# Performance work log

Hardware: AMD Instinct MI355X
Metric: run time of the kernel (lower is better)

## Reference

```python
import jax, jax.numpy as jnp
import numpy as np

HEAD_DIM = 128
MAX_TIMESCALE = 10000.0
MIN_TIMESCALE = 1.0


def _rope(x, pos):
    # x: [B, S, H, D], pos: [B, S]
    d = x.shape[-1]
    fraction = 2.0 * jnp.arange(0, d // 2, dtype=jnp.float32) / d
    timescale = MIN_TIMESCALE * (MAX_TIMESCALE / MIN_TIMESCALE) ** fraction  # [D/2]
    sinusoid = pos.astype(jnp.float32)[..., None, None] / timescale  # [B,S,1,D/2]
    sin, cos = jnp.sin(sinusoid), jnp.cos(sinusoid)
    xf = x.astype(jnp.float32)
    x1, x2 = jnp.split(xf, 2, axis=-1)
    return jnp.concatenate((x1 * cos - x2 * sin, x2 * cos + x1 * sin), axis=-1).astype(x.dtype)


def setup_inputs() -> dict:
    key = jax.random.key(0)
    ks = jax.random.split(key, 5)
    B, T, D, N, K, H = 2, 2048, 2048, 16, 4, HEAD_DIM
    s = 0.02
    X = jax.random.normal(ks[0], (B, T, D), dtype=jnp.float32)
    q_positions = jnp.broadcast_to(jnp.arange(T, dtype=jnp.int32), (B, T))
    Wq = jax.random.normal(ks[1], (D, N, H), dtype=jnp.float32) * s
    Wk = jax.random.normal(ks[2], (D, K, H), dtype=jnp.float32) * s
    Wv = jax.random.normal(ks[3], (D, K, H), dtype=jnp.float32) * s
    Wo = jax.random.normal(ks[4], (N, H, D), dtype=jnp.float32) * s
    return {"X": X, "q_positions": q_positions, "Wq": Wq, "Wk": Wk, "Wv": Wv, "Wo": Wo}


def reference(X, q_positions, Wq, Wk, Wv, Wo):
    B, T, D = X.shape
    N, K = Wq.shape[1], Wk.shape[1]
    groups = N // K
    # fused QKV projections (DenseGeneral, no bias)
    q = jnp.einsum('btd,dnh->btnh', X, Wq)  # [B,T,N,H]
    k = jnp.einsum('btd,dkh->btkh', X, Wk)  # [B,T,K,H]
    v = jnp.einsum('btd,dkh->btkh', X, Wv)  # [B,T,K,H]
    # RoPE (note: original uses q_positions sin/cos for both q and k in the no-cache path)
    q = _rope(q, q_positions)
    k = _rope(k, q_positions)
    # GQA: broadcast kv heads to query heads
    k = jnp.repeat(k, groups, axis=2)  # [B,T,N,H]
    v = jnp.repeat(v, groups, axis=2)
    # attention with scale=1.0 and causal masking
    scores = jnp.einsum('btnh,bsnh->bnts', q, k)  # [B,N,T,T]
    causal = jnp.tril(jnp.ones((T, T), dtype=bool))
    scores = jnp.where(causal, scores, jnp.finfo(scores.dtype).min)
    probs = jax.nn.softmax(scores, axis=-1)
    attn = jnp.einsum('bnts,bsnh->btnh', probs, v)  # [B,T,N,H]
    # output projection contracting (head, head_dim)
    out = jnp.einsum('btnh,nhd->btd', attn, Wo)
    return out.astype(X.dtype)
```

## Files before the change

kernel.cpp:

```cpp
#include <hip/hip_runtime.h>
#include <math.h>

#define DEVI static __device__ __forceinline__

using f16x8 = __attribute__((ext_vector_type(8))) _Float16;
using f32x4  = __attribute__((ext_vector_type(4))) float;

constexpr int Bb = 2, Tt = 2048, Dd = 2048, NQ = 16, NK = 4, HD = 128;
constexpr int Mrows = Bb * Tt;
constexpr int QKVC  = NQ*HD + 2*NK*HD;
constexpr int KOFF  = NQ*HD;
constexpr int VOFF  = NQ*HD + NK*HD;

DEVI ushort f2h(float f) {
  _Float16 h = (_Float16)f;
  union { _Float16 h; ushort u; } v; v.h = h;
  return v.u;
}
DEVI float h2f(ushort u) {
  union { ushort u; _Float16 h; } v; v.u = u;
  return (float)v.h;
}

typedef const __attribute__((address_space(1))) unsigned* gp1;
typedef __attribute__((address_space(3))) unsigned* lp3;
DEVI void gload16(void* lds, const void* g) {
  __builtin_amdgcn_global_load_lds((gp1)g, (lp3)lds, 16, 0, 0);
}

__global__ void k_cvt(const float* __restrict__ x, ushort* __restrict__ o, int n4) {
  int i = blockIdx.x * blockDim.x + threadIdx.x;
  if (i >= n4) return;
  float4 v = ((const float4*)x)[i];
  ushort4 u;
  u.x = f2h(v.x); u.y = f2h(v.y); u.z = f2h(v.z); u.w = f2h(v.w);
  ((ushort4*)o)[i] = u;
}

__global__ void k_tconv(const float* __restrict__ in, ushort* __restrict__ out, int R, int C) {
  __shared__ float t[32][33];
  const int c0 = blockIdx.x * 32, r0 = blockIdx.y * 32;
  const int tx = threadIdx.x, ty = threadIdx.y;
#pragma unroll
  for (int i = 0; i < 32; i += 8)
    t[ty + i][tx] = in[(size_t)(r0 + ty + i) * C + (c0 + tx)];
  __syncthreads();
#pragma unroll
  for (int i = 0; i < 32; i += 8)
    out[(size_t)(c0 + ty + i) * R + (r0 + tx)] = f2h(t[tx][ty + i]);
}

DEVI void stv(float* p, float v)  { *p = v; }
DEVI void stv(ushort* p, float v) { *p = f2h(v); }

template <typename OT>
__launch_bounds__(256)
__global__ void k_gemm_bt(const ushort* __restrict__ A, const ushort* __restrict__ Bt,
                          OT* __restrict__ C, int M, int N, int Kd) {
  __shared__ char As[8192];
  __shared__ char Bs[8192];
  const int tid = threadIdx.x;
  const int l = tid & 63, w = tid >> 6;
  const int wr = w >> 1, wc = w & 1;
  const int lr = l & 15, lk = l >> 4;
  const size_t row0 = (size_t)blockIdx.y * 128, col0 = (size_t)blockIdx.x * 128;

  f32x4 acc[4][4];
#pragma unroll
  for (int i = 0; i < 4; ++i)
#pragma unroll
    for (int j = 0; j < 4; ++j) acc[i][j] = (f32x4){0.f, 0.f, 0.f, 0.f};

  const int c0i = tid, c1i = tid + 256;
  const int ra0 = c0i >> 2, sa0 = (c0i & 3) ^ ((ra0 >> 1) & 3);
  const int ra1 = c1i >> 2, sa1 = (c1i & 3) ^ ((ra1 >> 1) & 3);

  for (int kt = 0; kt < Kd; kt += 32) {
    if (kt) __syncthreads();
    gload16(As + c0i * 16, A + (row0 + ra0) * Kd + kt + sa0 * 8);
    gload16(As + c1i * 16, A + (row0 + ra1) * Kd + kt + sa1 * 8);
    gload16(Bs + c0i * 16, Bt + (col0 + ra0) * Kd + kt + sa0 * 8);
    gload16(Bs + c1i * 16, Bt + (col0 + ra1) * Kd + kt + sa1 * 8);
    __syncthreads();
    f16x8 af[4], bfr[4];
#pragma unroll
    for (int i = 0; i < 4; ++i) {
      int ra = wr * 64 + i * 16 + lr;
      af[i] = *(const f16x8*)(As + ra * 64 + ((lk ^ ((ra >> 1) & 3)) << 4));
      int rb = wc * 64 + i * 16 + lr;
      bfr[i] = *(const f16x8*)(Bs + rb * 64 + ((lk ^ ((rb >> 1) & 3)) << 4));
    }
#pragma unroll
    for (int i = 0; i < 4; ++i)
#pragma unroll
      for (int j = 0; j < 4; ++j)
        acc[i][j] = __builtin_amdgcn_mfma_f32_16x16x32_f16(af[i], bfr[j], acc[i][j], 0, 0, 0);
  }
#pragma unroll
  for (int i = 0; i < 4; ++i) {
    size_t r = row0 + wr * 64 + i * 16 + lk * 4;
#pragma unroll
    for (int j = 0; j < 4; ++j) {
      size_t cc = col0 + wc * 64 + j * 16 + lr;
#pragma unroll
      for (int rg = 0; rg < 4; ++rg) stv(&C[(r + rg) * N + cc], acc[i][j][rg]);
    }
  }
}

__global__ void k_rope_tab(const int* __restrict__ pos, float* __restrict__ tab) {
  int idx = blockIdx.x * blockDim.x + threadIdx.x;
  if (idx >= Mrows * 64) return;
  int m = idx >> 6, i = idx & 63;
  double a = (double)pos[m] * exp2(-0.20762050593045952 * (double)i);
  tab[idx * 2]     = (float)cos(a);
  tab[idx * 2 + 1] = (float)sin(a);
}

__global__ void k_rope(ushort* __restrict__ qkv, const float* __restrict__ tab) {
  int idx = blockIdx.x * blockDim.x + threadIdx.x;
  if (idx >= Mrows * 20 * 8) return;
  int chunk = idx & 7;
  int h20 = (idx >> 3) % 20;
  int m = idx / 160;
  int colbase = (h20 < 16) ? h20 * 128 : (KOFF + (h20 - 16) * 128);
  size_t base = (size_t)m * QKVC + colbase + chunk * 8;
  union { uint4 v; ushort s[8]; } A1, A2, O1, O2;
  A1.v = *(const uint4*)(qkv + base);
  A2.v = *(const uint4*)(qkv + base + 64);
  const float* tp = tab + ((size_t)m * 64 + chunk * 8) * 2;
#pragma unroll
  for (int j = 0; j < 8; ++j) {
    float c = tp[2 * j], s = tp[2 * j + 1];
    float x1 = h2f(A1.s[j]), x2 = h2f(A2.s[j]);
    O1.s[j] = f2h(x1 * c - x2 * s);
    O2.s[j] = f2h(x2 * c + x1 * s);
  }
  *(uint4*)(qkv + base) = O1.v;
  *(uint4*)(qkv + base + 64) = O2.v;
}

__global__ void k_vt(const ushort* __restrict__ qkv, ushort* __restrict__ vt) {
  __shared__ ushort t[32][33];
  const int bg = blockIdx.z, bq = bg >> 2, g = bg & 3;
  const int s0 = blockIdx.x * 32, h0 = blockIdx.y * 32;
  const int tx = threadIdx.x, ty = threadIdx.y;
#pragma unroll
  for (int i = 0; i < 32; i += 8)
    t[ty + i][tx] = qkv[(size_t)(bq * Tt + s0 + ty + i) * QKVC + VOFF + g * HD + h0 + tx];
  __syncthreads();
#pragma unroll
  for (int i = 0; i < 32; i += 8)
    vt[((size_t)bg * HD + h0 + ty + i) * Tt + (s0 + tx)] = t[tx][ty + i];
}

__launch_bounds__(512, 4)
__global__ void k_flash(const ushort* __restrict__ qkv, const ushort* __restrict__ vt,
                        ushort* __restrict__ attn) {
  __shared__ char Ks[2][16384];
  __shared__ char Vs[2][16384];
  __shared__ char Pl[8][2048];
  const int b = blockIdx.x;
  const int vv = b >> 8, u = b & 255;
  const int hid = u >> 3, p = u & 7;
  const int qt = vv ? p : (15 - p);
  const int bq = hid >> 4, n = hid & 15, g = n >> 2;
  const int tid = threadIdx.x, w = tid >> 6, l = tid & 63;
  const int lr = l & 15, lk = l >> 4;
  const int t0 = qt * 128;
  const int qrow = t0 + w * 16;

  f16x8 qf[4];
  {
    const size_t qb = ((size_t)(bq * Tt + qrow + lr)) * QKVC + n * HD + lk * 8;
#pragma unroll
    for (int kt = 0; kt < 4; ++kt) qf[kt] = *(const f16x8*)(qkv + qb + kt * 32);
  }
  f32x4 O[8];
#pragma unroll
  for (int hb = 0; hb < 8; ++hb) O[hb] = (f32x4){0.f, 0.f, 0.f, 0.f};
  float mrow[4] = {-INFINITY, -INFINITY, -INFINITY, -INFINITY};
  float lrow[4] = {0.f, 0.f, 0.f, 0.f};

  const size_t kgbase = (size_t)(bq * Tt) * QKVC + KOFF + g * HD;
  const size_t vgbase = (size_t)(bq * 4 + g) * HD * Tt;
  const int ntiles = 2 * qt + 2;

  int srow[2], koin[2], hrow[2], voin[2];
#pragma unroll
  for (int cc = 0; cc < 2; ++cc) {
    int c = cc * 512 + tid;
    srow[cc] = c >> 4;
    koin[cc] = (((c & 15) << 4) ^ ((srow[cc] & 7) << 4)) >> 1;
    hrow[cc] = c >> 3;
    voin[cc] = (((c & 7) << 4) ^ ((hrow[cc] & 7) << 4)) >> 1;
  }

#define STAGE(buf, s0s)                                                              \
  {                                                                                  \
    _Pragma("unroll")                                                                \
    for (int cc = 0; cc < 2; ++cc) {                                                 \
      int c16 = (cc * 512 + tid) * 16;                                               \
      gload16(Ks[buf] + c16, qkv + kgbase + (size_t)((s0s) + srow[cc]) * QKVC + koin[cc]); \
      gload16(Vs[buf] + c16, vt + vgbase + (size_t)hrow[cc] * Tt + (s0s) + voin[cc]); \
    }                                                                                \
  }

  STAGE(0, 0);
  __syncthreads();

  for (int j = 0; j < ntiles; ++j) {
    const int cur = j & 1;
    if (j + 1 < ntiles) STAGE(cur ^ 1, (j + 1) * 64);
    const int s0 = j * 64;
    if (s0 <= qrow + 15) {
      f32x4 sc[4];
#pragma unroll
      for (int ns = 0; ns < 4; ++ns) {
        f32x4 a = (f32x4){0.f, 0.f, 0.f, 0.f};
        int sl = ns * 16 + lr;
#pragma unroll
        for (int kt = 0; kt < 4; ++kt) {
          int inner = (kt * 64 + lk * 16) ^ ((sl & 7) << 4);
          f16x8 kf = *(const f16x8*)(Ks[cur] + sl * 256 + inner);
          a = __builtin_amdgcn_mfma_f32_16x16x32_f16(qf[kt], kf, a, 0, 0, 0);
        }
        sc[ns] = a;
      }
      if (s0 + 63 > qrow) {
#pragma unroll
        for (int ns = 0; ns < 4; ++ns) {
          int scol = s0 + ns * 16 + lr;
#pragma unroll
          for (int r = 0; r < 4; ++r)
            if (scol > qrow + lk * 4 + r) sc[ns][r] = -INFINITY;
        }
      }
      float scl[4], rs[4];
#pragma unroll
      for (int r = 0; r < 4; ++r) {
        float v0 = fmaxf(fmaxf(sc[0][r], sc[1][r]), fmaxf(sc[2][r], sc[3][r]));
#pragma unroll
        for (int d = 1; d < 16; d <<= 1) v0 = fmaxf(v0, __shfl_xor(v0, d));
        float mn = fmaxf(mrow[r], v0);
        scl[r] = __expf(mrow[r] - mn);
        mrow[r] = mn;
        rs[r] = 0.f;
      }
#pragma unroll
      for (int ns = 0; ns < 4; ++ns)
#pragma unroll
        for (int r = 0; r < 4; ++r) {
          float pv = __expf(sc[ns][r] - mrow[r]);
          rs[r] += pv;
          int q = lk * 4 + r;
          *(ushort*)(Pl[w] + q * 128 + ((ns * 32 + lr * 2) ^ ((q & 7) << 4))) = f2h(pv);
        }
#pragma unroll
      for (int r = 0; r < 4; ++r) {
#pragma unroll
        for (int d = 1; d < 16; d <<= 1) rs[r] += __shfl_xor(rs[r], d);
        lrow[r] = lrow[r] * scl[r] + rs[r];
      }
#pragma unroll
      for (int hb = 0; hb < 8; ++hb)
#pragma unroll
        for (int r = 0; r < 4; ++r) O[hb][r] *= scl[r];
      const char* pb = Pl[w] + lr * 128;
      const int sw = (lr & 7) << 4;
      f16x8 pa0 = *(const f16x8*)(pb + ((lk * 16) ^ sw));
      f16x8 pa1 = *(const f16x8*)(pb + ((64 + lk * 16) ^ sw));
#pragma unroll
      for (int hb = 0; hb < 8; ++hb) {
        int h = hb * 16 + lr;
        int inner0 = (lk * 16) ^ ((h & 7) << 4);
        f16x8 vf0 = *(const f16x8*)(Vs[cur] + h * 128 + inner0);
        O[hb] = __builtin_amdgcn_mfma_f32_16x16x32_f16(pa0, vf0, O[hb], 0, 0, 0);
        int inner1 = (64 + lk * 16) ^ ((h & 7) << 4);
        f16x8 vf1 = *(const f16x8*)(Vs[cur] + h * 128 + inner1);
        O[hb] = __builtin_amdgcn_mfma_f32_16x16x32_f16(pa1, vf1, O[hb], 0, 0, 0);
      }
    }
    __syncthreads();
  }
#undef STAGE
  float inv[4];
#pragma unroll
  for (int r = 0; r < 4; ++r) inv[r] = 1.f / lrow[r];
#pragma unroll
  for (int hb = 0; hb < 8; ++hb)
#pragma unroll
    for (int r = 0; r < 4; ++r) {
      size_t orow = (size_t)(bq * Tt + qrow + lk * 4 + r);
      attn[orow * 2048 + n * HD + hb * 16 + lr] = f2h(O[hb][r] * inv[r]);
    }
}

extern "C" void kernel_launch(void* const* d_in, const int* in_sizes, int n_in,
                              void* d_out, int out_size, void* d_ws, size_t ws_size,
                              hipStream_t stream) {
  const float* X  = (const float*)d_in[0];
  const int*   qp = (const int*)d_in[1];
  const float* Wq = (const float*)d_in[2];
  const float* Wk = (const float*)d_in[3];
  const float* Wv = (const float*)d_in[4];
  const float* Wo = (const float*)d_in[5];
  float* out = (float*)d_out;
  char* ws = (char*)d_ws;

  ushort* Xf    = (ushort*)(ws + 0);
  ushort* WqkvT = (ushort*)(ws + 16777216);
  ushort* WoT   = (ushort*)(ws + 29360128);
  ushort* QKV   = (ushort*)(ws + 37748736);
  ushort* VT    = (ushort*)(ws + 62914560);
  ushort* attn  = (ushort*)(ws + 67108864);
  float*  tab   = (float*)(ws + 83886080);

  dim3 tb(32, 8);
  k_cvt<<<(Mrows * Dd / 4 + 255) / 256, 256, 0, stream>>>(X, Xf, Mrows * Dd / 4);
  k_tconv<<<dim3(64, 64), tb, 0, stream>>>(Wq, WqkvT, Dd, NQ * HD);
  k_tconv<<<dim3(16, 64), tb, 0, stream>>>(Wk, WqkvT + (size_t)KOFF * Dd, Dd, NK * HD);
  k_tconv<<<dim3(16, 64), tb, 0, stream>>>(Wv, WqkvT + (size_t)VOFF * Dd, Dd, NK * HD);
  k_tconv<<<dim3(64, 64), tb, 0, stream>>>(Wo, WoT, NQ * HD, Dd);
  k_gemm_bt<ushort><<<dim3(QKVC / 128, Mrows / 128), 256, 0, stream>>>(
      Xf, WqkvT, QKV, Mrows, QKVC, Dd);
  k_rope_tab<<<(Mrows * 64 + 255) / 256, 256, 0, stream>>>(qp, tab);
  k_rope<<<(Mrows * 160 + 255) / 256, 256, 0, stream>>>(QKV, tab);
  k_vt<<<dim3(Tt / 32, HD / 32, Bb * NK), tb, 0, stream>>>(QKV, VT);
  k_flash<<<dim3(512), 512, 0, stream>>>(QKV, VT, attn);
  k_gemm_bt<float><<<dim3(Dd / 128, Mrows / 128), 256, 0, stream>>>(
      attn, WoT, out, Mrows, Dd, Dd);
}
```

Baseline: 251.0 us.

## Transpose QK MFMA operands for lane-local softmax with lazy rescaling

Swaps the QK^T MFMA operands so each lane holds one query row's scores, which removes most of the cross-lane max and sum shuffles and allows packed fp16 stores of P into LDS. It adds a lazy online-softmax rescale that only updates the running max when a row's max grows by more than a threshold, so the O rescaling is usually skipped. It also adds s_setprio around the MFMA blocks and relaxes launch bounds from 4 to 2 waves per EU. The risks are lower occupancy and a round-toward-zero fp16 conversion of P with a stale max, where probabilities can reach up to e^8.

```diff
diff --git a/kernel.cpp b/kernel.cpp
--- a/kernel.cpp
+++ b/kernel.cpp
@@ -4,6 +4,7 @@
 #define DEVI static __device__ __forceinline__
 
 using f16x8 = __attribute__((ext_vector_type(8))) _Float16;
+using h16x2 = __attribute__((ext_vector_type(2))) __fp16;
 using f32x4  = __attribute__((ext_vector_type(4))) float;
 
 constexpr int Bb = 2, Tt = 2048, Dd = 2048, NQ = 16, NK = 4, HD = 128;
@@ -154,7 +155,7 @@
     vt[((size_t)bg * HD + h0 + ty + i) * Tt + (s0 + tx)] = t[tx][ty + i];
 }
 
-__launch_bounds__(512, 4)
+__launch_bounds__(512, 2)
 __global__ void k_flash(const ushort* __restrict__ qkv, const ushort* __restrict__ vt,
                         ushort* __restrict__ attn) {
   __shared__ char Ks[2][16384];
@@ -169,6 +170,7 @@
   const int lr = l & 15, lk = l >> 4;
   const int t0 = qt * 128;
   const int qrow = t0 + w * 16;
+  const int qglob = qrow + lr;
 
   f16x8 qf[4];
   {
@@ -179,8 +181,7 @@
   f32x4 O[8];
 #pragma unroll
   for (int hb = 0; hb < 8; ++hb) O[hb] = (f32x4){0.f, 0.f, 0.f, 0.f};
-  float mrow[4] = {-INFINITY, -INFINITY, -INFINITY, -INFINITY};
-  float lrow[4] = {0.f, 0.f, 0.f, 0.f};
+  float m = -INFINITY, lsum = 0.f;
 
   const size_t kgbase = (size_t)(bq * Tt) * QKVC + KOFF + g * HD;
   const size_t vgbase = (size_t)(bq * 4 + g) * HD * Tt;
@@ -215,6 +216,7 @@
     const int s0 = j * 64;
     if (s0 <= qrow + 15) {
       f32x4 sc[4];
+      __builtin_amdgcn_s_setprio(1);
 #pragma unroll
       for (int ns = 0; ns < 4; ++ns) {
         f32x4 a = (f32x4){0.f, 0.f, 0.f, 0.f};
@@ -223,53 +225,60 @@
         for (int kt = 0; kt < 4; ++kt) {
           int inner = (kt * 64 + lk * 16) ^ ((sl & 7) << 4);
           f16x8 kf = *(const f16x8*)(Ks[cur] + sl * 256 + inner);
-          a = __builtin_amdgcn_mfma_f32_16x16x32_f16(qf[kt], kf, a, 0, 0, 0);
+          a = __builtin_amdgcn_mfma_f32_16x16x32_f16(kf, qf[kt], a, 0, 0, 0);
         }
         sc[ns] = a;
       }
+      __builtin_amdgcn_s_setprio(0);
       if (s0 + 63 > qrow) {
 #pragma unroll
-        for (int ns = 0; ns < 4; ++ns) {
-          int scol = s0 + ns * 16 + lr;
+        for (int ns = 0; ns < 4; ++ns)
 #pragma unroll
           for (int r = 0; r < 4; ++r)
-            if (scol > qrow + lk * 4 + r) sc[ns][r] = -INFINITY;
-        }
-      }
-      float scl[4], rs[4];
-#pragma unroll
-      for (int r = 0; r < 4; ++r) {
-        float v0 = fmaxf(fmaxf(sc[0][r], sc[1][r]), fmaxf(sc[2][r], sc[3][r]));
-#pragma unroll
-        for (int d = 1; d < 16; d <<= 1) v0 = fmaxf(v0, __shfl_xor(v0, d));
-        float mn = fmaxf(mrow[r], v0);
-        scl[r] = __expf(mrow[r] - mn);
-        mrow[r] = mn;
-        rs[r] = 0.f;
-      }
+            if (s0 + ns * 16 + lk * 4 + r > qglob) sc[ns][r] = -INFINITY;
+      }
+      float pm = -INFINITY;
 #pragma unroll
       for (int ns = 0; ns < 4; ++ns)
-#pragma unroll
-        for (int r = 0; r < 4; ++r) {
-          float pv = __expf(sc[ns][r] - mrow[r]);
-          rs[r] += pv;
-          int q = lk * 4 + r;
-          *(ushort*)(Pl[w] + q * 128 + ((ns * 32 + lr * 2) ^ ((q & 7) << 4))) = f2h(pv);
-        }
-#pragma unroll
-      for (int r = 0; r < 4; ++r) {
-#pragma unroll
-        for (int d = 1; d < 16; d <<= 1) rs[r] += __shfl_xor(rs[r], d);
-        lrow[r] = lrow[r] * scl[r] + rs[r];
-      }
-#pragma unroll
-      for (int hb = 0; hb < 8; ++hb)
-#pragma unroll
-        for (int r = 0; r < 4; ++r) O[hb][r] *= scl[r];
-      const char* pb = Pl[w] + lr * 128;
-      const int sw = (lr & 7) << 4;
-      f16x8 pa0 = *(const f16x8*)(pb + ((lk * 16) ^ sw));
-      f16x8 pa1 = *(const f16x8*)(pb + ((64 + lk * 16) ^ sw));
+        pm = fmaxf(pm, fmaxf(fmaxf(sc[ns][0], sc[ns][1]), fmaxf(sc[ns][2], sc[ns][3])));
+      pm = fmaxf(pm, __shfl_xor(pm, 16));
+      pm = fmaxf(pm, __shfl_xor(pm, 32));
+      const bool doresc = !__all(pm - m <= 8.0f);
+      float scl = 1.f;
+      if (doresc) { float mn = fmaxf(m, pm); scl = __expf(m - mn); m = mn; }
+      float rs = 0.f;
+#pragma unroll
+      for (int ns = 0; ns < 4; ++ns) {
+#pragma unroll
+        for (int r = 0; r < 4; ++r) sc[ns][r] = __expf(sc[ns][r] - m);
+        rs += (sc[ns][0] + sc[ns][1]) + (sc[ns][2] + sc[ns][3]);
+      }
+      rs += __shfl_xor(rs, 16);
+      rs += __shfl_xor(rs, 32);
+      char* pwb = Pl[w] + lr * 128;
+      const int swz = (lr & 7) << 4;
+#pragma unroll
+      for (int ns = 0; ns < 4; ++ns) {
+        union { h16x2 h[2]; uint2 u; } pk;
+        pk.h[0] = __builtin_amdgcn_cvt_pkrtz(sc[ns][0], sc[ns][1]);
+        pk.h[1] = __builtin_amdgcn_cvt_pkrtz(sc[ns][2], sc[ns][3]);
+        *(uint2*)(pwb + ((ns * 32 + lk * 8) ^ swz)) = pk.u;
+      }
+      if (doresc) {
+        float sr[4];
+#pragma unroll
+        for (int r = 0; r < 4; ++r) sr[r] = __shfl(scl, lk * 4 + r);
+#pragma unroll
+        for (int hb = 0; hb < 8; ++hb)
+#pragma unroll
+          for (int r = 0; r < 4; ++r) O[hb][r] *= sr[r];
+        lsum = lsum * scl + rs;
+      } else {
+        lsum += rs;
+      }
+      f16x8 pa0 = *(const f16x8*)(pwb + ((lk * 16) ^ swz));
+      f16x8 pa1 = *(const f16x8*)(pwb + ((64 + lk * 16) ^ swz));
+      __builtin_amdgcn_s_setprio(1);
 #pragma unroll
       for (int hb = 0; hb < 8; ++hb) {
         int h = hb * 16 + lr;
@@ -280,19 +289,20 @@
         f16x8 vf1 = *(const f16x8*)(Vs[cur] + h * 128 + inner1);
         O[hb] = __builtin_amdgcn_mfma_f32_16x16x32_f16(pa1, vf1, O[hb], 0, 0, 0);
       }
+      __builtin_amdgcn_s_setprio(0);
     }
     __syncthreads();
   }
 #undef STAGE
-  float inv[4];
-#pragma unroll
-  for (int r = 0; r < 4; ++r) inv[r] = 1.f / lrow[r];
+  float iv[4];
+#pragma unroll
+  for (int r = 0; r < 4; ++r) iv[r] = 1.f / __shfl(lsum, lk * 4 + r);
 #pragma unroll
   for (int hb = 0; hb < 8; ++hb)
 #pragma unroll
     for (int r = 0; r < 4; ++r) {
       size_t orow = (size_t)(bq * Tt + qrow + lk * 4 + r);
-      attn[orow * 2048 + n * HD + hb * 16 + lr] = f2h(O[hb][r] * inv[r]);
+      attn[orow * 2048 + n * HD + hb * 16 + lr] = f2h(O[hb][r] * iv[r]);
     }
 }
 
```

New measurement: 216.8 us. 13.6% less time.
